# Kernel optimization log

Measured on AMD Instinct MI355X. Metric: run time of the kernel, lower is better.

Reference implementation:

```python
import jax, jax.numpy as jnp
import numpy as np

B, N, ND, ED = 4, 24, 13, 12          # batch, num_nodes, node feat dim, edge feat dim
H, NH, HD = 256, 8, 32                # hidden, heads, head dim (H == NH*HD)
L, T = 64, 1000                       # transformer layers, max_timestep
_SCALE = 1.0 / float(np.sqrt(H))      # torch divides by sqrt(node_dim)=sqrt(256)


def _ln(x, g, b):
    m = x.mean(-1, keepdims=True)
    v = ((x - m) ** 2).mean(-1, keepdims=True)
    return (x - m) / jnp.sqrt(v + 1e-5) * g + b


def setup_inputs() -> dict:
    key = jax.random.key(0)
    it = iter(jax.random.split(key, 40))
    def w(*s):
        return (jax.random.normal(next(it), s) * 0.02).astype(jnp.float32)
    z = lambda *s: jnp.zeros(s, jnp.float32)
    o = lambda *s: jnp.ones(s, jnp.float32)
    d = {}
    d['nodes'] = jax.random.normal(next(it), (B, N, ND), jnp.float32)
    d['edges'] = jax.random.normal(next(it), (B, N, N, ED), jnp.float32)
    d['conds'] = jax.random.randint(next(it), (B,), 0, T)
    # input MLPs
    d['inN_w1'] = w(ND, H); d['inN_b1'] = z(H); d['inN_w2'] = w(H, H); d['inN_b2'] = z(H)
    d['inE_w1'] = w(ED, H); d['inE_b1'] = z(H); d['inE_w2'] = w(H, H); d['inE_b2'] = z(H)
    d['inC_w1'] = w(T, H);  d['inC_b1'] = z(H); d['inC_w2'] = w(H, H); d['inC_b2'] = z(H)
    # stacked per-layer params (leading dim L, scanned)
    d['qkv_w'] = w(L, H, 3 * H); d['qkv_b'] = z(L, 3 * H)
    d['no_w'] = w(L, H, H); d['no_b'] = z(L, H)
    d['eo_w'] = w(L, H, H); d['eo_b'] = z(L, H)
    d['ln1n_g'] = o(L, H); d['ln1n_b'] = z(L, H)
    d['ln1e_g'] = o(L, H); d['ln1e_b'] = z(L, H)
    d['mn_w1'] = w(L, H, 4 * H); d['mn_b1'] = z(L, 4 * H)
    d['mn_w2'] = w(L, 4 * H, H); d['mn_b2'] = z(L, H)
    d['me_w1'] = w(L, H, 4 * H); d['me_b1'] = z(L, 4 * H)
    d['me_w2'] = w(L, 4 * H, H); d['me_b2'] = z(L, H)
    d['ln2n_g'] = o(L, H); d['ln2n_b'] = z(L, H)
    d['ln2e_g'] = o(L, H); d['ln2e_b'] = z(L, H)
    # output MLPs
    d['outN_w1'] = w(H, H); d['outN_b1'] = z(H); d['outN_w2'] = w(H, ND); d['outN_b2'] = z(ND)
    d['outE_w1'] = w(H, H); d['outE_b1'] = z(H); d['outE_w2'] = w(H, ED); d['outE_b2'] = z(ED)
    return d


def _forward(nodes, edges, conds,
             inN_w1, inN_b1, inN_w2, inN_b2, inE_w1, inE_b1, inE_w2, inE_b2,
             inC_w1, inC_b1, inC_w2, inC_b2,
             qkv_w, qkv_b, no_w, no_b, eo_w, eo_b,
             ln1n_g, ln1n_b, ln1e_g, ln1e_b,
             mn_w1, mn_b1, mn_w2, mn_b2, me_w1, me_b1, me_w2, me_b2,
             ln2n_g, ln2n_b, ln2e_g, ln2e_b,
             outN_w1, outN_b1, outN_w2, outN_b2, outE_w1, outE_b1, outE_w2, outE_b2):
    relu = jax.nn.relu
    c = jax.nn.one_hot(conds, T, dtype=nodes.dtype)
    c = relu(relu(c @ inC_w1 + inC_b1) @ inC_w2 + inC_b2)          # (B,H)
    n = relu(relu(nodes @ inN_w1 + inN_b1) @ inN_w2 + inN_b2)      # (B,N,H)
    e = relu(relu(edges @ inE_w1 + inE_b1) @ inE_w2 + inE_b2)      # (B,N,N,H)

    def layer(carry, p):
        n, e = carry
        (qw, qb, nw, nb, ew, eb, g1n, b1n, g1e, b1e,
         w1n, bb1n, w2n, bb2n, w1e, bb1e, w2e, bb2e, g2n, b2n, g2e, b2e) = p
        nc = n + c[:, None, :]
        q, k, v = jnp.split(nc @ qw + qb, 3, axis=-1)
        q = q.reshape(B, N, NH, HD); k = k.reshape(B, N, NH, HD); v = v.reshape(B, N, NH, HD)
        s5 = jnp.einsum('bihd,bjhd->bijhd', q, k) * _SCALE          # (B,N,N,NH,HD)
        ne5 = s5 + e.reshape(B, N, N, NH, HD)                       # edge-biased scores
        attn = jax.nn.softmax(ne5.sum(-1), axis=2)                  # (B,N,N,NH)
        wv = jnp.einsum('bijh,bjhd->bihd', attn, v).reshape(B, N, H)
        an = _ln(wv @ nw + nb + n, g1n, b1n)
        ae = _ln(relu(ne5.reshape(B, N, N, H) @ ew + eb) + e, g1e, b1e)
        n2 = _ln(relu(an @ w1n + bb1n) @ w2n + bb2n + an, g2n, b2n)
        e2 = _ln(relu(ae @ w1e + bb1e) @ w2e + bb2e + ae, g2e, b2e)
        return (n2, e2), None

    stacked = (qkv_w, qkv_b, no_w, no_b, eo_w, eo_b, ln1n_g, ln1n_b, ln1e_g, ln1e_b,
               mn_w1, mn_b1, mn_w2, mn_b2, me_w1, me_b1, me_w2, me_b2,
               ln2n_g, ln2n_b, ln2e_g, ln2e_b)
    (n, e), _ = jax.lax.scan(layer, (n, e), stacked)
    out_n = relu(n @ outN_w1 + outN_b1) @ outN_w2 + outN_b2
    out_e = relu(e @ outE_w1 + outE_b1) @ outE_w2 + outE_b2
    return out_n, out_e


def reference(nodes, edges, conds,
              inN_w1, inN_b1, inN_w2, inN_b2, inE_w1, inE_b1, inE_w2, inE_b2,
              inC_w1, inC_b1, inC_w2, inC_b2,
              qkv_w, qkv_b, no_w, no_b, eo_w, eo_b,
              ln1n_g, ln1n_b, ln1e_g, ln1e_b,
              mn_w1, mn_b1, mn_w2, mn_b2, me_w1, me_b1, me_w2, me_b2,
              ln2n_g, ln2n_b, ln2e_g, ln2e_b,
              outN_w1, outN_b1, outN_w2, outN_b2, outE_w1, outE_b1, outE_w2, outE_b2):
    return _forward(nodes, edges, conds,
                    inN_w1, inN_b1, inN_w2, inN_b2, inE_w1, inE_b1, inE_w2, inE_b2,
                    inC_w1, inC_b1, inC_w2, inC_b2,
                    qkv_w, qkv_b, no_w, no_b, eo_w, eo_b,
                    ln1n_g, ln1n_b, ln1e_g, ln1e_b,
                    mn_w1, mn_b1, mn_w2, mn_b2, me_w1, me_b1, me_w2, me_b2,
                    ln2n_g, ln2n_b, ln2e_g, ln2e_b,
                    outN_w1, outN_b1, outN_w2, outN_b2, outE_w1, outE_b1, outE_w2, outE_b2)
```

## Files before the change

### kernel.cpp

```cpp
#include <hip/hip_runtime.h>

typedef _Float16 half_t;
typedef _Float16 f16x8 __attribute__((ext_vector_type(8)));
typedef _Float16 f16x4 __attribute__((ext_vector_type(4)));
typedef float f32x4 __attribute__((ext_vector_type(4)));

#define BB 4
#define NNODE 24
#define NLAYER 64
#define SCALE_QK 0.0625f

#define WS_C     0
#define WS_N     1024
#define WS_NACC  25600
#define NACC_STRIDE 24576
#define WS_E     74752
#define WS_AE32  664576
#define WS_AE16  1254400
#define WS_AN16  1549312
#define WS_EPART 1561600
#define EPART_SLICE 589824
#define WS_WTF   3920896
#define SLOT_F16 1376256
#define OFF_QKVT 0
#define OFF_NOT  196608
#define OFF_EOT  262144
#define OFF_MN1T 327680
#define OFF_MN2T 589824
#define OFF_ME1T 851968
#define OFF_ME2T 1114112
#define OFF_INE2T  (3*SLOT_F16)
#define OFF_OUTE1T (3*SLOT_F16 + 65536)

struct Params {
  const float *nodes, *edges; const int* conds;
  const float *inN_w1,*inN_b1,*inN_w2,*inN_b2;
  const float *inE_w1,*inE_b1,*inE_w2,*inE_b2;
  const float *inC_w1,*inC_b1,*inC_w2,*inC_b2;
  const float *qkv_w,*qkv_b,*no_w,*no_b,*eo_w,*eo_b;
  const float *ln1n_g,*ln1n_b,*ln1e_g,*ln1e_b;
  const float *mn_w1,*mn_b1,*mn_w2,*mn_b2,*me_w1,*me_b1,*me_w2,*me_b2;
  const float *ln2n_g,*ln2n_b,*ln2e_g,*ln2e_b;
  const float *outN_w1,*outN_b1,*outN_w2,*outN_b2,*outE_w1,*outE_b1,*outE_w2,*outE_b2;
  float* ws; float* out;
};

template<int NT, int KS, int MT, int LDAH>
__device__ __forceinline__ void gemm_rs_acc(const half_t* __restrict__ WT, int ldb,
                                            const char* __restrict__ A,
                                            f32x4 (&acc)[NT][MT]) {
  const int lane = threadIdx.x & 63;
  const int wv = threadIdx.x >> 6;
  const int l15 = lane & 15;
  const int kg = lane >> 4;
  f16x8 b[NT][KS];
#pragma unroll
  for (int nt = 0; nt < NT; ++nt) {
    const int col = (nt * 8 + wv) * 16 + l15;
#pragma unroll
    for (int ks = 0; ks < KS; ++ks)
      b[nt][ks] = *(const f16x8*)(WT + (size_t)col * ldb + ks * 32 + kg * 8);
  }
#pragma unroll
  for (int m = 0; m < MT; ++m) {
    f16x8 a[KS];
    const int row = m * 16 + l15;
#pragma unroll
    for (int ks = 0; ks < KS; ++ks)
      a[ks] = *(const f16x8*)(A + row * (LDAH * 2) + (((ks * 32 + kg * 8) * 2) ^ ((row & 7) << 4)));
#pragma unroll
    for (int ks = 0; ks < KS; ++ks)
#pragma unroll
      for (int nt = 0; nt < NT; ++nt)
        acc[nt][m] = __builtin_amdgcn_mfma_f32_16x16x32_f16(a[ks], b[nt][ks], acc[nt][m], 0, 0, 0);
  }
}

template<int NT, int KS, int MT, int LDAH, typename EPI>
__device__ __forceinline__ void gemm_rs(const half_t* __restrict__ WT, int ldb,
                                        const char* __restrict__ A, EPI epi) {
  f32x4 acc[NT][MT];
#pragma unroll
  for (int nt = 0; nt < NT; ++nt)
#pragma unroll
    for (int m = 0; m < MT; ++m) {
      f32x4 z = {0.f, 0.f, 0.f, 0.f};
      acc[nt][m] = z;
    }
  gemm_rs_acc<NT, KS, MT, LDAH>(WT, ldb, A, acc);
#pragma unroll
  for (int nt = 0; nt < NT; ++nt)
#pragma unroll
    for (int m = 0; m < MT; ++m)
      epi(nt, m, acc[nt][m]);
}

template<int KS>
__device__ __forceinline__ void load_b1(const half_t* __restrict__ WT, int ldb, f16x8 (&b)[KS]) {
  const int lane = threadIdx.x & 63, wvq = threadIdx.x >> 6;
  const int col = wvq * 16 + (lane & 15), kg = lane >> 4;
#pragma unroll
  for (int ks = 0; ks < KS; ++ks)
    b[ks] = *(const f16x8*)(WT + (size_t)col * ldb + ks * 32 + kg * 8);
}

template<int KS, int MT, int LDAH, typename EPI>
__device__ __forceinline__ void gemm_rs_preb(const f16x8 (&b)[KS], const char* __restrict__ A, EPI epi) {
  const int lane = threadIdx.x & 63;
  const int l15 = lane & 15, kg = lane >> 4;
  f32x4 acc[MT];
#pragma unroll
  for (int m = 0; m < MT; ++m) { f32x4 z = {0.f,0.f,0.f,0.f}; acc[m] = z; }
#pragma unroll
  for (int m = 0; m < MT; ++m) {
    const int row = m * 16 + l15;
    f16x8 a[KS];
#pragma unroll
    for (int ks = 0; ks < KS; ++ks)
      a[ks] = *(const f16x8*)(A + row * (LDAH * 2) + (((ks * 32 + kg * 8) * 2) ^ ((row & 7) << 4)));
#pragma unroll
    for (int ks = 0; ks < KS; ++ks)
      acc[m] = __builtin_amdgcn_mfma_f32_16x16x32_f16(a[ks], b[ks], acc[m], 0, 0, 0);
  }
#pragma unroll
  for (int m = 0; m < MT; ++m) epi(m, acc[m]);
}

template<int NTW, int KT, int MT, int LDA, int LDB, typename EPI>
__device__ __forceinline__ void run_gemm_s(const half_t* __restrict__ WT,
                                           const char* __restrict__ A,
                                           EPI epi) {
  const int lane = threadIdx.x & 63;
  const int wv = threadIdx.x >> 6;
  const int l15 = lane & 15;
  const int kg = lane >> 4;
  constexpr int NC = KT / 8;
  constexpr int TC = NC * NTW;
  f16x8 bb[2][8];
  auto ldb = [&](int c, int w) {
    const int kc = c / NTW, n = c % NTW;
    const half_t* bp = WT + (size_t)((n * 8 + wv) * 16 + l15) * LDB + kc * 256 + kg * 8;
#pragma unroll
    for (int q = 0; q < 8; ++q) bb[w][q] = *(const f16x8*)(bp + q * 32);
  };
  f32x4 acc[NTW][MT];
#pragma unroll
  for (int n = 0; n < NTW; ++n)
#pragma unroll
    for (int m = 0; m < MT; ++m) {
      f32x4 z = {0.f, 0.f, 0.f, 0.f};
      acc[n][m] = z;
    }
  ldb(0, 0);
#pragma unroll
  for (int kc = 0; kc < NC; ++kc) {
    f16x8 a[8][MT];
#pragma unroll
    for (int q = 0; q < 8; ++q) {
      const int k0 = (kc * 8 + q) * 32 + kg * 8;
#pragma unroll
      for (int m = 0; m < MT; ++m) {
        const int row = m * 16 + l15;
        a[q][m] = *(const f16x8*)(A + row * (LDA * 2) + ((k0 * 2) ^ ((row & 7) << 4)));
      }
    }
#pragma unroll
    for (int n = 0; n < NTW; ++n) {
      const int c = kc * NTW + n;
      if (c + 1 < TC) ldb(c + 1, (c + 1) & 1);
#pragma unroll
      for (int q = 0; q < 8; ++q)
#pragma unroll
        for (int m = 0; m < MT; ++m)
          acc[n][m] = __builtin_amdgcn_mfma_f32_16x16x32_f16(a[q][m], bb[c & 1][q], acc[n][m], 0, 0, 0);
    }
  }
#pragma unroll
  for (int n = 0; n < NTW; ++n) epi(n, acc[n]);
}

__device__ void conv_matrix_tile(const float* __restrict__ src, half_t* __restrict__ dst,
                                 int K, int Nn, int tk, int tn, char* smem) {
  float* tl = (float*)smem;
  const int t = threadIdx.x;
  const int c = t & 63;
  const int r0 = t >> 6;
  for (int r = r0; r < 64; r += 8)
    tl[r * 65 + c] = src[(size_t)(tk * 64 + r) * Nn + tn * 64 + c];
  __syncthreads();
  for (int r = r0; r < 64; r += 8)
    dst[(size_t)(tn * 64 + r) * K + tk * 64 + c] = (half_t)tl[c * 65 + r];
  __syncthreads();
}

__device__ void conv_layer_tile(const Params& p, half_t* slot, int lw, int tile, char* smem) {
  if (tile < 48)       { conv_matrix_tile(p.qkv_w + (size_t)lw*196608, slot+OFF_QKVT, 256, 768, tile & 3, tile >> 2, smem); }
  else if (tile < 64)  { int t2 = tile-48;  conv_matrix_tile(p.no_w  + (size_t)lw*65536,  slot+OFF_NOT,  256, 256, t2 & 3,  t2 >> 2, smem); }
  else if (tile < 80)  { int t2 = tile-64;  conv_matrix_tile(p.eo_w  + (size_t)lw*65536,  slot+OFF_EOT,  256, 256, t2 & 3,  t2 >> 2, smem); }
  else if (tile < 144) { int t2 = tile-80;  conv_matrix_tile(p.mn_w1 + (size_t)lw*262144, slot+OFF_MN1T, 256, 1024, t2 & 3, t2 >> 2, smem); }
  else if (tile < 208) { int t2 = tile-144; conv_matrix_tile(p.mn_w2 + (size_t)lw*262144, slot+OFF_MN2T, 1024, 256, t2 & 15, t2 >> 4, smem); }
  else if (tile < 272) { int t2 = tile-208; conv_matrix_tile(p.me_w1 + (size_t)lw*262144, slot+OFF_ME1T, 256, 1024, t2 & 3, t2 >> 2, smem); }
  else                 { int t2 = tile-272; conv_matrix_tile(p.me_w2 + (size_t)lw*262144, slot+OFF_ME2T, 1024, 256, t2 & 15, t2 >> 4, smem); }
}

__global__ __launch_bounds__(512, 2) void k_embedA(Params p) {
  __shared__ __align__(16) char smem[17024];
  const int bid = blockIdx.x, tid = threadIdx.x;
  float* ws = p.ws;
  half_t* wt = (half_t*)(ws + WS_WTF);
  if (bid < 4) {
    const int b = bid;
    const int cond = p.conds[b];
    float* t1 = (float*)smem;
    if (tid < 256) t1[tid] = fmaxf(p.inC_w1[(size_t)cond * 256 + tid] + p.inC_b1[tid], 0.f);
    __syncthreads();
    if (tid < 256) {
      float s = p.inC_b2[tid];
      for (int k = 0; k < 256; ++k) s += t1[k] * p.inC_w2[(size_t)k * 256 + tid];
      ws[WS_C + b * 256 + tid] = fmaxf(s, 0.f);
    }
  } else {
    for (int job = bid - 4; job < 704; job += 128) {
      if (job < 336)      conv_layer_tile(p, wt, 0, job, smem);
      else if (job < 672) conv_layer_tile(p, wt + SLOT_F16, 1, job - 336, smem);
      else if (job < 688) { int t2 = job - 672; conv_matrix_tile(p.inE_w2,  wt + OFF_INE2T,  256, 256, t2 & 3, t2 >> 2, smem); }
      else                { int t2 = job - 688; conv_matrix_tile(p.outE_w1, wt + OFF_OUTE1T, 256, 256, t2 & 3, t2 >> 2, smem); }
    }
  }
}

__global__ __launch_bounds__(512, 2) void k_embedB(Params p) {
  __shared__ __align__(16) char smem[24640];
  const int bid = blockIdx.x, tid = threadIdx.x;
  const int lane = tid & 63, wv = tid >> 6, l15 = lane & 15, kg = lane >> 4;
  float* ws = p.ws;
  half_t* wt = (half_t*)(ws + WS_WTF);
  float* e0 = ws + WS_E;
  float* n0 = ws + WS_N;
  if (bid < 96) {
    const int b = bid / NNODE, i = bid % NNODE;
    float* eb = (float*)smem;
    char* t16 = smem + 2048;
    for (int idx = tid; idx < 24 * 12; idx += 512)
      eb[idx] = p.edges[((size_t)(b * NNODE + i) * NNODE + idx / 12) * 12 + idx % 12];
    __syncthreads();
    for (int idx = tid; idx < 32 * 32; idx += 512) {
      int r = idx >> 5, kb = idx & 31, k0 = kb * 8;
      f16x8 v;
#pragma unroll
      for (int j = 0; j < 8; ++j) v[j] = (half_t)0.f;
      if (r < NNODE) {
#pragma unroll
        for (int j = 0; j < 8; ++j) {
          int col = k0 + j;
          float s = p.inE_b1[col];
          for (int kk = 0; kk < 12; ++kk) s += eb[r * 12 + kk] * p.inE_w1[kk * 256 + col];
          v[j] = (half_t)fmaxf(s, 0.f);
        }
      }
      *(f16x8*)(t16 + r * 512 + ((k0 * 2) ^ ((r & 7) << 4))) = v;
    }
    __syncthreads();
    run_gemm_s<2, 8, 2, 256, 256>(wt + OFF_INE2T, t16,
      [&](int n, f32x4 (&accn)[2]) {
        const int col = (n * 8 + wv) * 16 + l15;
        const float bcol = p.inE_b2[col];
#pragma unroll
        for (int m = 0; m < 2; ++m)
#pragma unroll
          for (int r4 = 0; r4 < 4; ++r4) {
            const int row = m * 16 + kg * 4 + r4;
            if (row < NNODE)
              e0[((size_t)(b * NNODE + i) * NNODE + row) * 256 + col] = fmaxf(accn[m][r4] + bcol, 0.f);
          }
      });
  } else {
    const int nb = bid - 96, b = nb >> 1, hf = nb & 1, i0 = hf * 12;
    float* nd = (float*)smem;
    float* t1 = (float*)(smem + 1024);
    for (int idx = tid; idx < 12 * 13; idx += 512)
      nd[(idx / 13) * 16 + (idx % 13)] = p.nodes[(size_t)(b * NNODE + i0 + idx / 13) * 13 + idx % 13];
    __syncthreads();
    for (int idx = tid; idx < 12 * 256; idx += 512) {
      int r = idx >> 8, col = idx & 255;
      float s = p.inN_b1[col];
      for (int kk = 0; kk < 13; ++kk) s += nd[r * 16 + kk] * p.inN_w1[kk * 256 + col];
      t1[r * 257 + col] = fmaxf(s, 0.f);
    }
    __syncthreads();
    {
      int col = tid & 255, rh = tid >> 8;
      float a6[6] = {0.f, 0.f, 0.f, 0.f, 0.f, 0.f};
      for (int k = 0; k < 256; ++k) {
        float w = p.inN_w2[(size_t)k * 256 + col];
#pragma unroll
        for (int r = 0; r < 6; ++r) a6[r] += t1[(rh * 6 + r) * 257 + k] * w;
      }
#pragma unroll
      for (int r = 0; r < 6; ++r) {
        int row = rh * 6 + r;
        n0[(size_t)(b * NNODE + i0 + row) * 256 + col] = fmaxf(a6[r] + p.inN_b2[col], 0.f);
      }
    }
  }
}

__global__ __launch_bounds__(512, 2) void k_attn(Params p, int lyr) {
  __shared__ __align__(16) char smem[139488];
  const int bid = blockIdx.x, tid = threadIdx.x;
  const int lane = tid & 63, wv = tid >> 6, l15 = lane & 15, kg = lane >> 4;
  float* ws = p.ws;
  half_t* wt = (half_t*)(ws + WS_WTF);
  const half_t* slot = wt + (size_t)(lyr % 3) * SLOT_F16;

  if (bid >= 96) {
    if (lyr + 2 < NLAYER) {
      half_t* dslot = wt + (size_t)((lyr + 2) % 3) * SLOT_F16;
      for (int tile = bid - 96; tile < 336; tile += 126)
        conv_layer_tile(p, dslot, lyr + 2, tile, smem);
    }
    return;
  }
  const int b = bid / NNODE, i = bid % NNODE;
  const size_t rowbase = (size_t)(b * NNODE + i) * NNODE;
  char* nc16 = smem;
  half_t* qkv16 = (half_t*)(smem + 16384);
  char* ne5 = smem + 65536;
  float* e32 = (float*)(smem + 81920);
  float* psum = (float*)(smem + 106880);
  float* sc = (float*)(smem + 109952);
  float* wvl = (float*)(smem + 110720);
  float* ni = (float*)(smem + 111744);
  float* anr = (float*)(smem + 112768);
  float* aef = (float*)(smem + 114816);
  float* ae32 = ws + WS_AE32;
  half_t* ae16g = (half_t*)(ws + WS_AE16);
  const half_t* epart = (const half_t*)(ws + WS_EPART);
  const float* nacc_in = ws + WS_NACC + ((lyr + 1) & 1) * NACC_STRIDE;
  float* nacc_out = ws + WS_NACC + (lyr & 1) * NACC_STRIDE;
  const float* cb = ws + WS_C + b * 256;

  for (int r = wv; r < 32; r += 8) {
    const int c = lane * 4;
    f16x4 hv;
    if (r < NNODE) {
      f32x4 y;
      if (lyr == 0) {
        y = *(const f32x4*)(ws + WS_N + (size_t)(b * NNODE + r) * 256 + c);
      } else {
        f32x4 x = *(const f32x4*)(nacc_in + (size_t)(b * NNODE + r) * 256 + c);
        float s = x[0] + x[1] + x[2] + x[3];
        float s2 = x[0]*x[0] + x[1]*x[1] + x[2]*x[2] + x[3]*x[3];
#pragma unroll
        for (int off = 32; off; off >>= 1) { s += __shfl_xor(s, off); s2 += __shfl_xor(s2, off); }
        float mean = s * (1.f / 256.f);
        float rstd = rsqrtf(s2 * (1.f / 256.f) - mean * mean + 1e-5f);
        const float* g = p.ln2n_g + (size_t)(lyr - 1) * 256;
        const float* bv = p.ln2n_b + (size_t)(lyr - 1) * 256;
#pragma unroll
        for (int j = 0; j < 4; ++j) y[j] = (x[j] - mean) * rstd * g[c + j] + bv[c + j];
      }
      if (r == i) *(f32x4*)(ni + c) = y;
#pragma unroll
      for (int j = 0; j < 4; ++j) hv[j] = (half_t)(y[j] + cb[c + j]);
    } else {
#pragma unroll
      for (int j = 0; j < 4; ++j) hv[j] = (half_t)0.f;
    }
    *(f16x4*)(nc16 + r * 512 + ((lane * 8) ^ ((r & 7) << 4))) = hv;
  }
  __syncthreads();
  {
    const float* qb = p.qkv_b + (size_t)lyr * 768;
#pragma unroll
    for (int h2 = 0; h2 < 2; ++h2) {
      gemm_rs<3, 8, 2, 256>(slot + OFF_QKVT + (size_t)(h2 * 384) * 256, 256, nc16,
        [&](int nt, int m, f32x4 v) {
          const int gcol = h2 * 384 + (nt * 8 + wv) * 16 + l15;
          const float bc = qb[gcol];
#pragma unroll
          for (int r4 = 0; r4 < 4; ++r4) {
            const int row = m * 16 + kg * 4 + r4;
            qkv16[(size_t)row * 768 + gcol] = (half_t)(v[r4] + bc);
          }
        });
    }
  }
  __syncthreads();
  for (int idx = tid; idx < 32 * 32; idx += 512) {
    int r = idx >> 5, kb = idx & 31, k0 = kb * 8;
    f16x8 v;
#pragma unroll
    for (int j = 0; j < 8; ++j) v[j] = (half_t)0.f;
    if (r < NNODE) {
      const size_t row = rowbase + r;
      float x[8];
      if (lyr == 0) {
        const f32x4 a = *(const f32x4*)(ws + WS_E + row * 256 + k0);
        const f32x4 b4 = *(const f32x4*)(ws + WS_E + row * 256 + k0 + 4);
#pragma unroll
        for (int j = 0; j < 4; ++j) { x[j] = a[j]; x[4 + j] = b4[j]; }
      } else {
        const float* mb2 = p.me_b2 + (size_t)(lyr - 1) * 256;
        const f32x4 a = *(const f32x4*)(ae32 + row * 256 + k0);
        const f32x4 b4 = *(const f32x4*)(ae32 + row * 256 + k0 + 4);
#pragma unroll
        for (int j = 0; j < 4; ++j) { x[j] = a[j] + mb2[k0 + j]; x[4 + j] = b4[j] + mb2[k0 + 4 + j]; }
#pragma unroll
        for (int hb = 0; hb < 8; ++hb) {
          f16x8 pv = *(const f16x8*)(epart + (size_t)hb * EPART_SLICE + row * 256 + k0);
#pragma unroll
          for (int j = 0; j < 8; ++j) x[j] += (float)pv[j];
        }
        float s = 0.f, s2 = 0.f;
#pragma unroll
        for (int j = 0; j < 8; ++j) { s += x[j]; s2 += x[j] * x[j]; }
#pragma unroll
        for (int off = 16; off; off >>= 1) { s += __shfl_xor(s, off); s2 += __shfl_xor(s2, off); }
        float mean = s * (1.f / 256.f);
        float rstd = rsqrtf(s2 * (1.f / 256.f) - mean * mean + 1e-5f);
        const float* g = p.ln2e_g + (size_t)(lyr - 1) * 256;
        const float* bv = p.ln2e_b + (size_t)(lyr - 1) * 256;
#pragma unroll
        for (int j = 0; j < 8; ++j) x[j] = (x[j] - mean) * rstd * g[k0 + j] + bv[k0 + j];
      }
      f16x8 q8 = *(const f16x8*)(qkv16 + (size_t)i * 768 + k0);
      f16x8 k8 = *(const f16x8*)(qkv16 + (size_t)r * 768 + 256 + k0);
      float ps = 0.f;
#pragma unroll
      for (int j = 0; j < 8; ++j) {
        float f = SCALE_QK * (float)q8[j] * (float)k8[j] + x[j];
        v[j] = (half_t)f;
        ps += f;
        e32[r * 260 + k0 + j] = x[j];
      }
      psum[r * 32 + kb] = ps;
    }
    *(f16x8*)(ne5 + r * 512 + ((k0 * 2) ^ ((r & 7) << 4))) = v;
  }
  __syncthreads();
  if (tid < 192) {
    int hq = tid & 7;
    sc[tid] = psum[(tid >> 3) * 32 + hq * 4] + psum[(tid >> 3) * 32 + hq * 4 + 1] +
              psum[(tid >> 3) * 32 + hq * 4 + 2] + psum[(tid >> 3) * 32 + hq * 4 + 3];
  }
  __syncthreads();
  if (tid < 256) {
    const int h = tid >> 5, j = tid & 31;
    float v = (j < 24) ? sc[j * 8 + h] : -1e30f;
    float mx = v;
#pragma unroll
    for (int off = 16; off; off >>= 1) mx = fmaxf(mx, __shfl_xor(mx, off));
    float ex = (j < 24) ? __expf(v - mx) : 0.f;
    float sum = ex;
#pragma unroll
    for (int off = 16; off; off >>= 1) sum += __shfl_xor(sum, off);
    if (j < 24) sc[j * 8 + h] = ex / sum;
  }
  __syncthreads();
  if (tid < 256) {
    const int d = tid, h = d >> 5;
    float a = 0.f;
#pragma unroll
    for (int j = 0; j < 24; ++j) a += sc[j * 8 + h] * (float)qkv16[(size_t)j * 768 + 512 + d];
    wvl[d] = a;
  }
  {
    const float* eob = p.eo_b + (size_t)lyr * 256;
    gemm_rs<2, 8, 2, 256>(slot + OFF_EOT, 256, ne5,
      [&](int nt, int m, f32x4 v) {
        const int col = (nt * 8 + wv) * 16 + l15;
#pragma unroll
        for (int r4 = 0; r4 < 4; ++r4) {
          const int row = m * 16 + kg * 4 + r4;
          if (row < NNODE)
            aef[row * 257 + col] = fmaxf(v[r4] + eob[col], 0.f) + e32[row * 260 + col];
        }
      });
  }
  __syncthreads();
  {
    const float* g = p.ln1e_g + (size_t)lyr * 256;
    const float* bv = p.ln1e_b + (size_t)lyr * 256;
    for (int r = wv; r < NNODE; r += 8) {
      float x[4];
#pragma unroll
      for (int j = 0; j < 4; ++j) x[j] = aef[r * 257 + lane * 4 + j];
      float s = x[0] + x[1] + x[2] + x[3];
      float s2 = x[0]*x[0] + x[1]*x[1] + x[2]*x[2] + x[3]*x[3];
#pragma unroll
      for (int off = 32; off; off >>= 1) { s += __shfl_xor(s, off); s2 += __shfl_xor(s2, off); }
      float mean = s * (1.f / 256.f);
      float rstd = rsqrtf(s2 * (1.f / 256.f) - mean * mean + 1e-5f);
      f16x4 hv; f32x4 yv;
#pragma unroll
      for (int j = 0; j < 4; ++j) {
        int c = lane * 4 + j;
        float y = (x[j] - mean) * rstd * g[c] + bv[c];
        yv[j] = y; hv[j] = (half_t)y;
      }
      *(f32x4*)(ae32 + (rowbase + r) * 256 + lane * 4) = yv;
      *(f16x4*)(ae16g + (rowbase + r) * 256 + lane * 4) = hv;
    }
  }
  {
    const half_t* NOT_ = slot + OFF_NOT;
    int c = tid & 255, hf = tid >> 8;
    float s = 0.f;
    const half_t* wp = NOT_ + (size_t)c * 256 + hf * 128;
#pragma unroll
    for (int k8 = 0; k8 < 16; ++k8) {
      f16x8 w8 = *(const f16x8*)(wp + k8 * 8);
#pragma unroll
      for (int j = 0; j < 8; ++j) s += wvl[hf * 128 + k8 * 8 + j] * (float)w8[j];
    }
    anr[hf * 256 + c] = s;
  }
  __syncthreads();
  if (wv == 0) {
    const float* nob = p.no_b + (size_t)lyr * 256;
    const float* g = p.ln1n_g + (size_t)lyr * 256;
    const float* bv = p.ln1n_b + (size_t)lyr * 256;
    const float* mb2 = p.mn_b2 + (size_t)lyr * 256;
    float x[4];
#pragma unroll
    for (int j = 0; j < 4; ++j) {
      int c = lane * 4 + j;
      x[j] = anr[c] + anr[256 + c] + nob[c] + ni[c];
    }
    float s = x[0] + x[1] + x[2] + x[3];
    float s2 = x[0]*x[0] + x[1]*x[1] + x[2]*x[2] + x[3]*x[3];
#pragma unroll
    for (int off = 32; off; off >>= 1) { s += __shfl_xor(s, off); s2 += __shfl_xor(s2, off); }
    float mean = s * (1.f / 256.f);
    float rstd = rsqrtf(s2 * (1.f / 256.f) - mean * mean + 1e-5f);
    f16x4 hv; f32x4 av;
#pragma unroll
    for (int j = 0; j < 4; ++j) {
      int c = lane * 4 + j;
      float y = (x[j] - mean) * rstd * g[c] + bv[c];
      hv[j] = (half_t)y;
      av[j] = y + mb2[c];
    }
    *(f16x4*)((half_t*)(ws + WS_AN16) + (size_t)(b * NNODE + i) * 256 + lane * 4) = hv;
    *(f32x4*)(nacc_out + (size_t)(b * NNODE + i) * 256 + lane * 4) = av;
  }
}

__global__ __launch_bounds__(512, 2) void k_mlp(Params p, int lyr) {
  __shared__ __align__(16) char smem[73728];
  const int bid = blockIdx.x, tid = threadIdx.x;
  const int lane = tid & 63, wv = tid >> 6, l15 = lane & 15, kg = lane >> 4;
  float* ws = p.ws;
  half_t* wt = (half_t*)(ws + WS_WTF);
  const half_t* slot = wt + (size_t)(lyr % 3) * SLOT_F16;

  if (bid < 192) {
    const int rb = bid >> 3, hb = bid & 7;
    const int row0 = rb * 96;
    char* A16 = smem;
    char* hl = smem + 49152;
    f16x8 b1[8];
    load_b1<8>(slot + OFF_ME1T + (size_t)(hb * 128) * 256, 256, b1);
    const half_t* aeg = (const half_t*)(ws + WS_AE16) + (size_t)row0 * 256;
    for (int idx = tid; idx < 96 * 32; idx += 512) {
      int r = idx >> 5, c8 = idx & 31;
      f16x8 v = *(const f16x8*)(aeg + r * 256 + c8 * 8);
      *(f16x8*)(A16 + r * 512 + ((c8 * 16) ^ ((r & 7) << 4))) = v;
    }
    __syncthreads();
    const float* mb1 = p.me_b1 + (size_t)lyr * 1024 + hb * 128;
    gemm_rs_preb<8, 6, 256>(b1, A16,
      [&](int m, f32x4 v) {
        const int colb = wv * 16 + l15;
        const float bc = mb1[colb];
#pragma unroll
        for (int r4 = 0; r4 < 4; ++r4) {
          const int row = m * 16 + kg * 4 + r4;
          *(half_t*)(hl + row * 256 + ((colb * 2) ^ ((row & 7) << 4))) = (half_t)fmaxf(v[r4] + bc, 0.f);
        }
      });
    __syncthreads();
    half_t* ep = (half_t*)(ws + WS_EPART) + (size_t)hb * EPART_SLICE + (size_t)row0 * 256;
    gemm_rs<2, 4, 6, 128>(slot + OFF_ME2T + hb * 128, 1024, hl,
      [&](int nt, int m, f32x4 v) {
        const int col = (nt * 8 + wv) * 16 + l15;
#pragma unroll
        for (int r4 = 0; r4 < 4; ++r4)
          ep[(size_t)(m * 16 + kg * 4 + r4) * 256 + col] = (half_t)v[r4];
      });
  } else {
    const int hb = bid - 192;
    char* A16 = smem;
    char* hl = smem + 49152;
    f16x8 b1[8];
    load_b1<8>(slot + OFF_MN1T + (size_t)(hb * 128) * 256, 256, b1);
    const half_t* ang = (const half_t*)(ws + WS_AN16);
    for (int idx = tid; idx < 96 * 32; idx += 512) {
      int r = idx >> 5, c8 = idx & 31;
      f16x8 v = *(const f16x8*)(ang + (size_t)r * 256 + c8 * 8);
      *(f16x8*)(A16 + r * 512 + ((c8 * 16) ^ ((r & 7) << 4))) = v;
    }
    __syncthreads();
    const float* mb1 = p.mn_b1 + (size_t)lyr * 1024 + hb * 128;
    gemm_rs_preb<8, 6, 256>(b1, A16,
      [&](int m, f32x4 v) {
        const int colb = wv * 16 + l15;
        const float bc = mb1[colb];
#pragma unroll
        for (int r4 = 0; r4 < 4; ++r4) {
          const int row = m * 16 + kg * 4 + r4;
          *(half_t*)(hl + row * 256 + ((colb * 2) ^ ((row & 7) << 4))) = (half_t)fmaxf(v[r4] + bc, 0.f);
        }
      });
    __syncthreads();
    float* nacc_out = ws + WS_NACC + (lyr & 1) * NACC_STRIDE;
    gemm_rs<2, 4, 6, 128>(slot + OFF_MN2T + hb * 128, 1024, hl,
      [&](int nt, int m, f32x4 v) {
        const int col = (nt * 8 + wv) * 16 + l15;
#pragma unroll
        for (int r4 = 0; r4 < 4; ++r4)
          atomicAdd(&nacc_out[(size_t)(m * 16 + kg * 4 + r4) * 256 + col], v[r4]);
      });
  }
}

__global__ __launch_bounds__(512, 2) void k_out(Params p) {
  __shared__ __align__(16) char smem[49472];
  const int bid = blockIdx.x, tid = threadIdx.x;
  const int lane = tid & 63, wv = tid >> 6, l15 = lane & 15, kg = lane >> 4;
  float* ws = p.ws;
  half_t* wt = (half_t*)(ws + WS_WTF);
  const float* ae32 = ws + WS_AE32;
  const half_t* epart = (const half_t*)(ws + WS_EPART);
  if (bid < 96) {
    const int b = bid / NNODE, i = bid % NNODE;
    const size_t rowbase = (size_t)(b * NNODE + i) * NNODE;
    char* A16 = smem;
    float* h2f = (float*)(smem + 16384);
    const float* mb2 = p.me_b2 + (size_t)63 * 256;
    const float* g = p.ln2e_g + (size_t)63 * 256;
    const float* bvv = p.ln2e_b + (size_t)63 * 256;
    for (int idx = tid; idx < 32 * 32; idx += 512) {
      int r = idx >> 5, kb = idx & 31, k0 = kb * 8;
      f16x8 v;
#pragma unroll
      for (int j = 0; j < 8; ++j) v[j] = (half_t)0.f;
      if (r < NNODE) {
        const size_t row = rowbase + r;
        float x[8];
        const f32x4 a = *(const f32x4*)(ae32 + row * 256 + k0);
        const f32x4 b4 = *(const f32x4*)(ae32 + row * 256 + k0 + 4);
#pragma unroll
        for (int j = 0; j < 4; ++j) { x[j] = a[j] + mb2[k0 + j]; x[4 + j] = b4[j] + mb2[k0 + 4 + j]; }
#pragma unroll
        for (int hb = 0; hb < 8; ++hb) {
          f16x8 pv = *(const f16x8*)(epart + (size_t)hb * EPART_SLICE + row * 256 + k0);
#pragma unroll
          for (int j = 0; j < 8; ++j) x[j] += (float)pv[j];
        }
        float s = 0.f, s2 = 0.f;
#pragma unroll
        for (int j = 0; j < 8; ++j) { s += x[j]; s2 += x[j] * x[j]; }
#pragma unroll
        for (int off = 16; off; off >>= 1) { s += __shfl_xor(s, off); s2 += __shfl_xor(s2, off); }
        float mean = s * (1.f / 256.f);
        float rstd = rsqrtf(s2 * (1.f / 256.f) - mean * mean + 1e-5f);
#pragma unroll
        for (int j = 0; j < 8; ++j)
          v[j] = (half_t)((x[j] - mean) * rstd * g[k0 + j] + bvv[k0 + j]);
      }
      *(f16x8*)(A16 + r * 512 + ((k0 * 2) ^ ((r & 7) << 4))) = v;
    }
    __syncthreads();
    run_gemm_s<2, 8, 2, 256, 256>(wt + OFF_OUTE1T, A16,
      [&](int n, f32x4 (&accn)[2]) {
        const int col = (n * 8 + wv) * 16 + l15;
#pragma unroll
        for (int m = 0; m < 2; ++m)
#pragma unroll
          for (int r4 = 0; r4 < 4; ++r4) {
            const int row = m * 16 + kg * 4 + r4;
            h2f[row * 257 + col] = (row < NNODE) ? fmaxf(accn[m][r4] + p.outE_b1[col], 0.f) : 0.f;
          }
      });
    __syncthreads();
    for (int pr = tid; pr < 24 * 12; pr += 512) {
      int j = pr / 12, oc = pr % 12;
      float s = p.outE_b2[oc];
      for (int k = 0; k < 256; ++k) s += h2f[j * 257 + k] * p.outE_w2[k * 12 + oc];
      p.out[1248 + ((size_t)(b * NNODE + i) * NNODE + j) * 12 + oc] = s;
    }
  } else {
    const int nb = bid - 96, bq = nb >> 1, hf = nb & 1, i0 = hf * 12;
    float* nl = (float*)smem;
    float* t1f = (float*)(smem + 12544);
    const float* n_acc = ws + WS_NACC + 1 * NACC_STRIDE;
    const float* g = p.ln2n_g + (size_t)63 * 256;
    const float* bvv = p.ln2n_b + (size_t)63 * 256;
    for (int r = wv; r < 12; r += 8) {
      const int row = bq * NNODE + i0 + r;
      const int c = lane * 4;
      f32x4 x = *(const f32x4*)(n_acc + (size_t)row * 256 + c);
      float s = x[0] + x[1] + x[2] + x[3];
      float s2 = x[0]*x[0] + x[1]*x[1] + x[2]*x[2] + x[3]*x[3];
#pragma unroll
      for (int off = 32; off; off >>= 1) { s += __shfl_xor(s, off); s2 += __shfl_xor(s2, off); }
      float mean = s * (1.f / 256.f);
      float rstd = rsqrtf(s2 * (1.f / 256.f) - mean * mean + 1e-5f);
      f32x4 y;
#pragma unroll
      for (int j = 0; j < 4; ++j) y[j] = (x[j] - mean) * rstd * g[c + j] + bvv[c + j];
      *(f32x4*)(nl + r * 257 + c) = y;
    }
    __syncthreads();
    {
      int col = tid & 255, rh = tid >> 8;
      float a6[6] = {0.f, 0.f, 0.f, 0.f, 0.f, 0.f};
      for (int k = 0; k < 256; ++k) {
        float w = p.outN_w1[(size_t)k * 256 + col];
#pragma unroll
        for (int r = 0; r < 6; ++r) a6[r] += nl[(rh * 6 + r) * 257 + k] * w;
      }
#pragma unroll
      for (int r = 0; r < 6; ++r)
        t1f[(rh * 6 + r) * 257 + col] = fmaxf(a6[r] + p.outN_b1[col], 0.f);
    }
    __syncthreads();
    for (int pr = tid; pr < 12 * 13; pr += 512) {
      int il = pr / 13, oc = pr % 13;
      float s = p.outN_b2[oc];
      for (int k = 0; k < 256; ++k) s += t1f[il * 257 + k] * p.outN_w2[k * 13 + oc];
      p.out[((size_t)(bq * NNODE) + i0 + il) * 13 + oc] = s;
    }
  }
}

extern "C" void kernel_launch(void* const* d_in, const int* in_sizes, int n_in,
                              void* d_out, int out_size, void* d_ws, size_t ws_size,
                              hipStream_t stream) {
  (void)in_sizes; (void)n_in; (void)out_size; (void)ws_size;
  Params p;
  const float* const* fi = (const float* const*)d_in;
  p.nodes = fi[0]; p.edges = fi[1]; p.conds = (const int*)d_in[2];
  p.inN_w1 = fi[3]; p.inN_b1 = fi[4]; p.inN_w2 = fi[5]; p.inN_b2 = fi[6];
  p.inE_w1 = fi[7]; p.inE_b1 = fi[8]; p.inE_w2 = fi[9]; p.inE_b2 = fi[10];
  p.inC_w1 = fi[11]; p.inC_b1 = fi[12]; p.inC_w2 = fi[13]; p.inC_b2 = fi[14];
  p.qkv_w = fi[15]; p.qkv_b = fi[16]; p.no_w = fi[17]; p.no_b = fi[18];
  p.eo_w = fi[19]; p.eo_b = fi[20];
  p.ln1n_g = fi[21]; p.ln1n_b = fi[22]; p.ln1e_g = fi[23]; p.ln1e_b = fi[24];
  p.mn_w1 = fi[25]; p.mn_b1 = fi[26]; p.mn_w2 = fi[27]; p.mn_b2 = fi[28];
  p.me_w1 = fi[29]; p.me_b1 = fi[30]; p.me_w2 = fi[31]; p.me_b2 = fi[32];
  p.ln2n_g = fi[33]; p.ln2n_b = fi[34]; p.ln2e_g = fi[35]; p.ln2e_b = fi[36];
  p.outN_w1 = fi[37]; p.outN_b1 = fi[38]; p.outN_w2 = fi[39]; p.outN_b2 = fi[40];
  p.outE_w1 = fi[41]; p.outE_b1 = fi[42]; p.outE_w2 = fi[43]; p.outE_b2 = fi[44];
  p.ws = (float*)d_ws; p.out = (float*)d_out;

  k_embedA<<<dim3(132), dim3(512), 0, stream>>>(p);
  k_embedB<<<dim3(104), dim3(512), 0, stream>>>(p);
  for (int l = 0; l < NLAYER; ++l) {
    k_attn<<<dim3(222), dim3(512), 0, stream>>>(p, l);
    k_mlp<<<dim3(200), dim3(512), 0, stream>>>(p, l);
  }
  k_out<<<dim3(104), dim3(512), 0, stream>>>(p);
}
```

Measured before the change: 3.014 ms.

## Accumulate edge MLP partials with fp32 atomics into ping-pong buffer instead of fp16 slices

Edge MLP second-layer partial sums, one per hidden-dim block, are now atomically added into a double-buffered fp32 accumulator. That buffer is pre-seeded with the residual plus the me_b2 bias. Previously they were written as eight fp16 slices that the next layer had to read and sum. This removes the 8-slice reduction reads and shrinks workspace traffic, at the cost of many global float atomics with possible contention. The QKV projection is also split into three 256-column GEMM passes instead of two 384-column passes.

```diff
diff --git a/kernel.cpp b/kernel.cpp
--- a/kernel.cpp
+++ b/kernel.cpp
@@ -15,12 +15,11 @@
 #define WS_NACC  25600
 #define NACC_STRIDE 24576
 #define WS_E     74752
-#define WS_AE32  664576
-#define WS_AE16  1254400
-#define WS_AN16  1549312
-#define WS_EPART 1561600
-#define EPART_SLICE 589824
-#define WS_WTF   3920896
+#define WS_EACC  664576
+#define EACC_STRIDE 589824
+#define WS_AE16  1844224
+#define WS_AN16  2139136
+#define WS_WTF   2151424
 #define SLOT_F16 1376256
 #define OFF_QKVT 0
 #define OFF_NOT  196608
@@ -333,9 +332,9 @@
   float* ni = (float*)(smem + 111744);
   float* anr = (float*)(smem + 112768);
   float* aef = (float*)(smem + 114816);
-  float* ae32 = ws + WS_AE32;
   half_t* ae16g = (half_t*)(ws + WS_AE16);
-  const half_t* epart = (const half_t*)(ws + WS_EPART);
+  const float* eacc_in = ws + WS_EACC + ((lyr + 1) & 1) * EACC_STRIDE;
+  float* eacc_out = ws + WS_EACC + (lyr & 1) * EACC_STRIDE;
   const float* nacc_in = ws + WS_NACC + ((lyr + 1) & 1) * NACC_STRIDE;
   float* nacc_out = ws + WS_NACC + (lyr & 1) * NACC_STRIDE;
   const float* cb = ws + WS_C + b * 256;
@@ -373,10 +372,10 @@
   {
     const float* qb = p.qkv_b + (size_t)lyr * 768;
 #pragma unroll
-    for (int h2 = 0; h2 < 2; ++h2) {
-      gemm_rs<3, 8, 2, 256>(slot + OFF_QKVT + (size_t)(h2 * 384) * 256, 256, nc16,
+    for (int nn = 0; nn < 3; ++nn) {
+      gemm_rs<2, 8, 2, 256>(slot + OFF_QKVT + (size_t)(nn * 256) * 256, 256, nc16,
         [&](int nt, int m, f32x4 v) {
-          const int gcol = h2 * 384 + (nt * 8 + wv) * 16 + l15;
+          const int gcol = nn * 256 + (nt * 8 + wv) * 16 + l15;
           const float bc = qb[gcol];
 #pragma unroll
           for (int r4 = 0; r4 < 4; ++r4) {
@@ -401,17 +400,10 @@
 #pragma unroll
         for (int j = 0; j < 4; ++j) { x[j] = a[j]; x[4 + j] = b4[j]; }
       } else {
-        const float* mb2 = p.me_b2 + (size_t)(lyr - 1) * 256;
-        const f32x4 a = *(const f32x4*)(ae32 + row * 256 + k0);
-        const f32x4 b4 = *(const f32x4*)(ae32 + row * 256 + k0 + 4);
-#pragma unroll
-        for (int j = 0; j < 4; ++j) { x[j] = a[j] + mb2[k0 + j]; x[4 + j] = b4[j] + mb2[k0 + 4 + j]; }
-#pragma unroll
-        for (int hb = 0; hb < 8; ++hb) {
-          f16x8 pv = *(const f16x8*)(epart + (size_t)hb * EPART_SLICE + row * 256 + k0);
-#pragma unroll
-          for (int j = 0; j < 8; ++j) x[j] += (float)pv[j];
-        }
+        const f32x4 a = *(const f32x4*)(eacc_in + row * 256 + k0);
+        const f32x4 b4 = *(const f32x4*)(eacc_in + row * 256 + k0 + 4);
+#pragma unroll
+        for (int j = 0; j < 4; ++j) { x[j] = a[j]; x[4 + j] = b4[j]; }
         float s = 0.f, s2 = 0.f;
 #pragma unroll
         for (int j = 0; j < 8; ++j) { s += x[j]; s2 += x[j] * x[j]; }
@@ -482,6 +474,7 @@
   {
     const float* g = p.ln1e_g + (size_t)lyr * 256;
     const float* bv = p.ln1e_b + (size_t)lyr * 256;
+    const float* mb2e = p.me_b2 + (size_t)lyr * 256;
     for (int r = wv; r < NNODE; r += 8) {
       float x[4];
 #pragma unroll
@@ -492,14 +485,15 @@
       for (int off = 32; off; off >>= 1) { s += __shfl_xor(s, off); s2 += __shfl_xor(s2, off); }
       float mean = s * (1.f / 256.f);
       float rstd = rsqrtf(s2 * (1.f / 256.f) - mean * mean + 1e-5f);
-      f16x4 hv; f32x4 yv;
+      f16x4 hv; f32x4 ev;
 #pragma unroll
       for (int j = 0; j < 4; ++j) {
         int c = lane * 4 + j;
         float y = (x[j] - mean) * rstd * g[c] + bv[c];
-        yv[j] = y; hv[j] = (half_t)y;
-      }
-      *(f32x4*)(ae32 + (rowbase + r) * 256 + lane * 4) = yv;
+        ev[j] = y + mb2e[c];
+        hv[j] = (half_t)y;
+      }
+      *(f32x4*)(eacc_out + (rowbase + r) * 256 + lane * 4) = ev;
       *(f16x4*)(ae16g + (rowbase + r) * 256 + lane * 4) = hv;
     }
   }
@@ -581,13 +575,13 @@
         }
       });
     __syncthreads();
-    half_t* ep = (half_t*)(ws + WS_EPART) + (size_t)hb * EPART_SLICE + (size_t)row0 * 256;
+    float* ea = ws + WS_EACC + (lyr & 1) * EACC_STRIDE + (size_t)row0 * 256;
     gemm_rs<2, 4, 6, 128>(slot + OFF_ME2T + hb * 128, 1024, hl,
       [&](int nt, int m, f32x4 v) {
         const int col = (nt * 8 + wv) * 16 + l15;
 #pragma unroll
         for (int r4 = 0; r4 < 4; ++r4)
-          ep[(size_t)(m * 16 + kg * 4 + r4) * 256 + col] = (half_t)v[r4];
+          atomicAdd(&ea[(size_t)(m * 16 + kg * 4 + r4) * 256 + col], v[r4]);
       });
   } else {
     const int hb = bid - 192;
@@ -631,14 +625,12 @@
   const int lane = tid & 63, wv = tid >> 6, l15 = lane & 15, kg = lane >> 4;
   float* ws = p.ws;
   half_t* wt = (half_t*)(ws + WS_WTF);
-  const float* ae32 = ws + WS_AE32;
-  const half_t* epart = (const half_t*)(ws + WS_EPART);
+  const float* eacc = ws + WS_EACC + 1 * EACC_STRIDE;
   if (bid < 96) {
     const int b = bid / NNODE, i = bid % NNODE;
     const size_t rowbase = (size_t)(b * NNODE + i) * NNODE;
     char* A16 = smem;
     float* h2f = (float*)(smem + 16384);
-    const float* mb2 = p.me_b2 + (size_t)63 * 256;
     const float* g = p.ln2e_g + (size_t)63 * 256;
     const float* bvv = p.ln2e_b + (size_t)63 * 256;
     for (int idx = tid; idx < 32 * 32; idx += 512) {
@@ -649,16 +641,10 @@
       if (r < NNODE) {
         const size_t row = rowbase + r;
         float x[8];
-        const f32x4 a = *(const f32x4*)(ae32 + row * 256 + k0);
-        const f32x4 b4 = *(const f32x4*)(ae32 + row * 256 + k0 + 4);
-#pragma unroll
-        for (int j = 0; j < 4; ++j) { x[j] = a[j] + mb2[k0 + j]; x[4 + j] = b4[j] + mb2[k0 + 4 + j]; }
-#pragma unroll
-        for (int hb = 0; hb < 8; ++hb) {
-          f16x8 pv = *(const f16x8*)(epart + (size_t)hb * EPART_SLICE + row * 256 + k0);
-#pragma unroll
-          for (int j = 0; j < 8; ++j) x[j] += (float)pv[j];
-        }
+        const f32x4 a = *(const f32x4*)(eacc + row * 256 + k0);
+        const f32x4 b4 = *(const f32x4*)(eacc + row * 256 + k0 + 4);
+#pragma unroll
+        for (int j = 0; j < 4; ++j) { x[j] = a[j]; x[4 + j] = b4[j]; }
         float s = 0.f, s2 = 0.f;
 #pragma unroll
         for (int j = 0; j < 8; ++j) { s += x[j]; s2 += x[j] * x[j]; }
```

Result: slower. 3.431 ms (+13.8%).
